# Performance work log

Measured on AMD Instinct MI355X. Metric: run time of the kernel, lower is better.

Reference implementation:

```python
import jax, jax.numpy as jnp
import numpy as np

N_GRAM = 3
N_HEAD = 8


def setup_inputs() -> dict:
    key = jax.random.key(0)
    ks = jax.random.split(key, 8)
    V, E, H, H2, C, B, L = 50000, 512, 512, 512, 10, 64, 512
    def rn(k, shape, scale):
        return jax.random.normal(k, shape, jnp.float32) * jnp.float32(scale)
    return {
        "x": jax.random.randint(ks[0], (B, L), 0, V),
        "emb": rn(ks[1], (V, E), 0.02),
        "Wq": rn(ks[2], (H, E), 1.0 / np.sqrt(H)),
        "Wx": rn(ks[3], (E, 3 * H), 1.0 / np.sqrt(E)),
        "Wh": rn(ks[4], (H, 3 * H), 1.0 / np.sqrt(H)),
        "bx": jnp.zeros((3 * H,), jnp.float32),
        "bh": jnp.zeros((3 * H,), jnp.float32),
        "W1": rn(ks[5], (H, H2), 1.0 / np.sqrt(H)),
        "b1": jnp.zeros((H2,), jnp.float32),
        "W2": rn(ks[6], (H2, C), 1.0 / np.sqrt(H2)),
        "b2": jnp.zeros((C,), jnp.float32),
    }


def _gru_ngram_attn(xe, Wq, Wx, Wh, bx, bh):
    # xe: [B, L, E] embedded sequence
    B, L, E = xe.shape
    g, nh = N_GRAM, N_HEAD
    hd = E // nh
    H = Wh.shape[0]
    scale = jnp.float32(1.0 / np.sqrt(hd))
    xpad = jnp.pad(xe, ((0, 0), (g - 1, 0), (0, 0)))
    win = jnp.stack([xpad[:, i:i + L] for i in range(g)], axis=2)  # [B,L,g,E]
    win_t = jnp.transpose(win, (1, 0, 2, 3))  # [L,B,g,E] for scan
    h0 = jnp.zeros((B, H), xe.dtype)

    def step(h, w):
        # multi-head dot attention: query from prev hidden, keys/values = n-gram window
        q = (h @ Wq).reshape(B, nh, hd)          # [B,nh,hd]
        k = w.reshape(B, g, nh, hd)              # [B,g,nh,hd]
        scores = jnp.einsum('bnd,bgnd->bng', q, k) * scale
        a = jax.nn.softmax(scores, axis=-1)      # over window positions
        ctx = jnp.einsum('bng,bgnd->bnd', a, k).reshape(B, E)
        # GRU cell with attended context as input
        gx = ctx @ Wx + bx
        gh = h @ Wh + bh
        xr, xz, xn = jnp.split(gx, 3, axis=-1)
        hr, hz, hn = jnp.split(gh, 3, axis=-1)
        r = jax.nn.sigmoid(xr + hr)
        z = jax.nn.sigmoid(xz + hz)
        n = jnp.tanh(xn + r * hn)
        hnew = (1.0 - z) * n + z * h
        return hnew, hnew

    _, hs = jax.lax.scan(step, h0, win_t)  # [L,B,H]
    return hs


def reference(x, emb, Wq, Wx, Wh, bx, bh, W1, b1, W2, b2):
    xe = emb[x]  # [B,L,E]
    hs = _gru_ngram_attn(xe, Wq, Wx, Wh, bx, bh)  # [L,B,H]
    pooled = jax.nn.relu(hs.sum(axis=0))          # sum over seq, then relu
    out = pooled @ W1 + b1                        # fc1 path (H != embed not needed; H is GRU out)
    out = out @ W2 + b2                           # [B,C]
    return out
```

## Files before the change

kernel.cpp:

```cpp
#include <hip/hip_runtime.h>
#include <hip/hip_fp16.h>

typedef __attribute__((ext_vector_type(2))) _Float16 half2v;
typedef __attribute__((ext_vector_type(2))) __fp16   fp16x2;

#define SEQ     512
#define THREADS 512

#define WQ_OFF   0
#define WX_OFF   32768
#define WH_OFF   131072
#define SYNC_OFF 3670016

__device__ inline unsigned int pack2f16(float a, float b) {
    fp16x2 p = __builtin_amdgcn_cvt_pkrtz(a, b);
    return __builtin_bit_cast(unsigned int, p);
}
__device__ inline float fdot2u(unsigned int a, unsigned int b, float acc) {
    return __builtin_amdgcn_fdot2(__builtin_bit_cast(half2v, a),
                                  __builtin_bit_cast(half2v, b), acc, false);
}
__device__ inline float dot4(uint4 h, uint4 w, float acc) {
    acc = fdot2u(h.x, w.x, acc); acc = fdot2u(h.y, w.y, acc);
    acc = fdot2u(h.z, w.z, acc); acc = fdot2u(h.w, w.w, acc);
    return acc;
}
__device__ inline float fsigmoid(float x) { return 1.f / (1.f + __expf(-x)); }
__device__ inline float ftanhf(float x) {
    float e = __expf(-2.f * fabsf(x));
    float t = (1.f - e) / (1.f + e);
    return copysignf(t, x);
}
__device__ inline void vmem_fence() { asm volatile("s_waitcnt vmcnt(0)" ::: "memory"); }
__device__ inline unsigned a_ld(unsigned* p) {
    return __hip_atomic_load(p, __ATOMIC_RELAXED, __HIP_MEMORY_SCOPE_AGENT);
}
__device__ inline void a_st(unsigned* p, unsigned v) {
    __hip_atomic_store(p, v, __ATOMIC_RELAXED, __HIP_MEMORY_SCOPE_AGENT);
}
__device__ inline float a_ldf(float* p) {
    return __hip_atomic_load(p, __ATOMIC_RELAXED, __HIP_MEMORY_SCOPE_AGENT);
}
__device__ inline void a_stf(float* p, float v) {
    __hip_atomic_store(p, v, __ATOMIC_RELAXED, __HIP_MEMORY_SCOPE_AGENT);
}

__global__ __launch_bounds__(256)
void pack_weights(const float* __restrict__ Wq,
                  const float* __restrict__ Wx,
                  const float* __restrict__ Wh,
                  uint4* __restrict__ ws) {
    int tid = blockIdx.x * blockDim.x + threadIdx.x;
    const float* src; uint4* dst; int C, idx;
    if (tid < 64 * 512)                  { src = Wq; dst = ws;          C = 512;  idx = tid; }
    else if (tid < 64 * 512 + 64 * 1536) { src = Wx; dst = ws + WX_OFF; C = 1536; idx = tid - 64 * 512; }
    else                                 { src = Wh; dst = ws + WH_OFF; C = 1536; idx = tid - (64 * 512 + 64 * 1536); }
    int m4 = idx / C;
    int c  = idx - m4 * C;
    const float* s = src + (size_t)(m4 * 8) * C + c;
    uint4 o;
    o.x = pack2f16(s[0 * (size_t)C], s[1 * (size_t)C]);
    o.y = pack2f16(s[2 * (size_t)C], s[3 * (size_t)C]);
    o.z = pack2f16(s[4 * (size_t)C], s[5 * (size_t)C]);
    o.w = pack2f16(s[6 * (size_t)C], s[7 * (size_t)C]);
    dst[idx] = o;
}

__global__ __launch_bounds__(THREADS)
void gru_scan(const int* __restrict__ xtok, const float* __restrict__ emb,
              const uint4* __restrict__ wsp, const float* __restrict__ bx,
              const float* __restrict__ bh, const float* __restrict__ W1,
              const float* __restrict__ b1, const float* __restrict__ W2,
              const float* __restrict__ b2, float* __restrict__ out)
{
    const int blk  = blockIdx.x;
    const int gid  = blk & 7;
    const int bid  = blk >> 3;
    const int tid  = threadIdx.x;
    const int lane = tid & 63;
    const int wid  = tid >> 6;
    const int colsub = lane & 7;
    const int bp     = (lane >> 3) & 3;
    const int chsub  = lane >> 5;

    char* syncb = (char*)wsp + SYNC_OFF;
    unsigned* flagH = (unsigned*)syncb;
    unsigned* flagS = (unsigned*)(syncb + 1024);
    unsigned* Hbuf  = (unsigned*)(syncb + 2048);
    float* Pbuf     = (float*)(syncb + 133120);
    float* pooled_g = (float*)(syncb + 182272);
    float* fc1_g    = (float*)(syncb + 313344);

    __shared__ uint4 lds_W [64][65];
    __shared__ uint4 lds_Wx[64][49];
    __shared__ uint4 lds_h4[8][65];
    __shared__ unsigned u_pk[3][8][48][4];
    __shared__ float redQf[1152];
    __shared__ float redH[8][48][9];
    __shared__ float a_all[8][8][3];

    for (int i = tid; i < 64 * 64; i += THREADS) {
        int ch = i >> 6, cl = i & 63;
        uint4 v;
        if (cl < 16) v = wsp[WQ_OFF + ch * 512 + bid * 16 + cl];
        else { int g = (cl - 16) >> 4, c = (cl - 16) & 15;
               v = wsp[WH_OFF + ch * 1536 + g * 512 + bid * 16 + c]; }
        lds_W[ch][cl] = v;
    }
    for (int i = tid; i < 64 * 48; i += THREADS) {
        int ch = i / 48, cl = i - ch * 48;
        int g = cl >> 4, c = cl & 15;
        lds_Wx[ch][cl] = wsp[WX_OFF + ch * 1536 + g * 512 + bid * 16 + c];
    }

    float bxr = 0, bxz = 0, bxn = 0, bhr = 0, bhz = 0, bhn = 0;
    if (tid < 128) {
        int c = tid >> 3, cg = bid * 16 + c;
        bxr = bx[cg]; bxz = bx[512 + cg]; bxn = bx[1024 + cg];
        bhr = bh[cg]; bhz = bh[512 + cg]; bhn = bh[1024 + cg];
    }

    const int gb = gid * 8 + wid;
    {
        int tk = xtok[gb * SEQ];
        const float4* p = (const float4*)(emb + (size_t)tk * 512 + lane * 8);
        float4 ra = p[0], rb = p[1];
        uint4 pk;
        pk.x = pack2f16(ra.x, ra.y); pk.y = pack2f16(ra.z, ra.w);
        pk.z = pack2f16(rb.x, rb.y); pk.w = pack2f16(rb.z, rb.w);
        lds_h4[wid][lane] = pk;
        unsigned* up = &u_pk[0][0][0][0];
        for (int i = tid; i < 3072; i += THREADS) up[1536 + i] = 0u;
    }
    float hprev = 0.f, pooledv = 0.f;
    __syncthreads();

    for (int t = 0; t < SEQ; ++t) {
        const int par = t & 1;
        const int slot = t % 3;

        int tnext = (t + 1 < SEQ) ? (t + 1) : t;
        int tkn = xtok[gb * SEQ + tnext];
        const float4* pn = (const float4*)(emb + (size_t)tkn * 512 + lane * 8);
        float4 r3a = pn[0], r3b = pn[1];

        float winv[16];
        int b3 = 0, g3 = 0, trow = -1;
        if (wid == 0 && lane < 24) {
            b3 = lane / 3; g3 = lane - b3 * 3;
            trow = t - 2 + g3;
            int tok = (trow >= 0) ? xtok[(gid * 8 + b3) * SEQ + trow] : -1;
            if (tok >= 0) {
                const float* er = emb + (size_t)tok * 512 + bid * 16;
                #pragma unroll
                for (int d = 0; d < 16; ++d) winv[d] = er[d];
            } else {
                #pragma unroll
                for (int d = 0; d < 16; ++d) winv[d] = 0.f;
            }
        }

        {
            float acu[12];
            #pragma unroll
            for (int i = 0; i < 12; ++i) acu[i] = 0.f;
            int ch0 = wid * 8 + chsub * 4;
            #pragma unroll
            for (int i = 0; i < 4; ++i) {
                int ch = ch0 + i;
                uint4 c0 = lds_h4[bp][ch], c1 = lds_h4[bp + 4][ch];
                #pragma unroll
                for (int j = 0; j < 6; ++j) {
                    uint4 w = lds_Wx[ch][colsub + 8 * j];
                    acu[j]     = dot4(c0, w, acu[j]);
                    acu[6 + j] = dot4(c1, w, acu[6 + j]);
                }
            }
            #pragma unroll
            for (int i = 0; i < 12; ++i) acu[i] += __shfl_xor(acu[i], 32);
            if (chsub == 0) {
                #pragma unroll
                for (int j = 0; j < 6; ++j)
                    u_pk[slot][wid][colsub + 8 * j][bp] = pack2f16(acu[j], acu[6 + j]);
            }
        }

        if (wid == 0) {
            bool done = lane >= 32;
            while (!__all(done)) {
                if (!done) done = (a_ld(&flagH[gid * 32 + lane]) >= (unsigned)t);
                if (!__all(done)) __builtin_amdgcn_s_sleep(1);
            }
        }
        __syncthreads();

        {
            int bb = tid >> 6, c4 = tid & 63;
            unsigned* s = Hbuf + (size_t)(par ^ 1) * 16384 + (gid * 8 + bb) * 256 + c4 * 4;
            uint4 v;
            v.x = a_ld(s); v.y = a_ld(s + 1); v.z = a_ld(s + 2); v.w = a_ld(s + 3);
            lds_h4[bb][c4] = v;
        }
        __syncthreads();

        {
            float aq0 = 0, aq1 = 0, aq2 = 0, aq3 = 0;
            int ch0 = wid * 8 + chsub * 4;
            #pragma unroll
            for (int i = 0; i < 4; ++i) {
                int ch = ch0 + i;
                uint4 h0 = lds_h4[bp][ch], h1 = lds_h4[bp + 4][ch];
                uint4 w0 = lds_W[ch][colsub], w1 = lds_W[ch][colsub + 8];
                aq0 = dot4(h0, w0, aq0); aq1 = dot4(h0, w1, aq1);
                aq2 = dot4(h1, w0, aq2); aq3 = dot4(h1, w1, aq3);
            }
            aq0 += __shfl_xor(aq0, 32); aq1 += __shfl_xor(aq1, 32);
            aq2 += __shfl_xor(aq2, 32); aq3 += __shfl_xor(aq3, 32);
            if (chsub == 0) {
                redQf[(wid * 16 + colsub) * 9 + bp]         = aq0;
                redQf[(wid * 16 + colsub + 8) * 9 + bp]     = aq1;
                redQf[(wid * 16 + colsub) * 9 + bp + 4]     = aq2;
                redQf[(wid * 16 + colsub + 8) * 9 + bp + 4] = aq3;
            }
        }
        __syncthreads();

        if (wid == 0) {
            if (lane < 24) {
                float s = 0.f;
                if (trow >= 0) {
                    #pragma unroll
                    for (int d = 0; d < 16; ++d) {
                        float q = redQf[d * 9 + b3];
                        #pragma unroll
                        for (int k = 1; k < 8; ++k) q += redQf[(k * 16 + d) * 9 + b3];
                        s += winv[d] * q;
                    }
                }
                a_stf(&Pbuf[(size_t)((par * 8 + gid) * 32 + bid) * 24 + b3 * 3 + g3], s);
            }
            vmem_fence();
            if (lane == 0) a_st(&flagS[gid * 32 + bid], (unsigned)(t + 1));
            bool done = lane >= 32;
            while (!__all(done)) {
                if (!done) done = (a_ld(&flagS[gid * 32 + lane]) >= (unsigned)(t + 1));
                if (!__all(done)) __builtin_amdgcn_s_sleep(1);
            }
            {
                int bb = lane >> 3, n = lane & 7;
                float* pb = Pbuf + (size_t)(par * 8 + gid) * 32 * 24;
                float sc0 = 0, sc1 = 0, sc2 = 0;
                #pragma unroll
                for (int j = 0; j < 4; ++j) {
                    float* pj = pb + (n * 4 + j) * 24 + bb * 3;
                    sc0 += a_ldf(pj); sc1 += a_ldf(pj + 1); sc2 += a_ldf(pj + 2);
                }
                sc0 *= 0.125f; sc1 *= 0.125f; sc2 *= 0.125f;
                float mx = fmaxf(sc0, fmaxf(sc1, sc2));
                float e0 = __expf(sc0 - mx), e1 = __expf(sc1 - mx), e2 = __expf(sc2 - mx);
                float inv = 1.f / (e0 + e1 + e2);
                a_all[bb][n][0] = e0 * inv; a_all[bb][n][1] = e1 * inv; a_all[bb][n][2] = e2 * inv;
            }
        } else {
            #pragma unroll 1
            for (int rep = 0; rep < 2; ++rep) {
                int k = (rep == 0) ? wid : 0;
                if (rep == 1 && wid != 7) break;
                float ag[12];
                #pragma unroll
                for (int i = 0; i < 12; ++i) ag[i] = 0.f;
                int ch0 = k * 8 + chsub * 4;
                #pragma unroll
                for (int i = 0; i < 4; ++i) {
                    int ch = ch0 + i;
                    uint4 h0 = lds_h4[bp][ch], h1 = lds_h4[bp + 4][ch];
                    #pragma unroll
                    for (int j = 0; j < 6; ++j) {
                        uint4 w = lds_W[ch][16 + colsub + 8 * j];
                        ag[j]     = dot4(h0, w, ag[j]);
                        ag[6 + j] = dot4(h1, w, ag[6 + j]);
                    }
                }
                #pragma unroll
                for (int i = 0; i < 12; ++i) ag[i] += __shfl_xor(ag[i], 32);
                if (chsub == 0) {
                    #pragma unroll
                    for (int j = 0; j < 6; ++j) {
                        redH[k][colsub + 8 * j][bp]     = ag[j];
                        redH[k][colsub + 8 * j][bp + 4] = ag[6 + j];
                    }
                }
            }
        }
        __syncthreads();

        if (tid >= 64 && tid < 448) {
            int idx = tid - 64;
            int col = idx >> 3, bb = idx & 7;
            float ghs = redH[0][col][bb];
            #pragma unroll
            for (int k = 1; k < 8; ++k) ghs += redH[k][col][bb];
            float gxs = 0.f;
            int half = bb >> 2, bq = bb & 3;
            #pragma unroll
            for (int g = 0; g < 3; ++g) {
                int sg = (t + 1 + g) % 3;
                #pragma unroll
                for (int k = 0; k < 8; ++k) {
                    fp16x2 uv = __builtin_bit_cast(fp16x2, u_pk[sg][k][col][bq]);
                    gxs += a_all[bb][k][g] * (float)uv[half];
                }
            }
            redQf[col * 8 + bb]       = ghs;
            redQf[384 + col * 8 + bb] = gxs;
        }
        {
            uint4 pk;
            pk.x = pack2f16(r3a.x, r3a.y); pk.y = pack2f16(r3a.z, r3a.w);
            pk.z = pack2f16(r3b.x, r3b.y); pk.w = pack2f16(r3b.z, r3b.w);
            lds_h4[wid][lane] = pk;
        }
        __syncthreads();

        if (tid < 128) {
            int c = tid >> 3, bb = tid & 7;
            float ghr = redQf[c * 8 + bb]        + bhr;
            float ghz = redQf[(16 + c) * 8 + bb] + bhz;
            float ghn = redQf[(32 + c) * 8 + bb] + bhn;
            float gxr = redQf[384 + c * 8 + bb]        + bxr;
            float gxz = redQf[384 + (16 + c) * 8 + bb] + bxz;
            float gxn = redQf[384 + (32 + c) * 8 + bb] + bxn;
            float r = fsigmoid(gxr + ghr);
            float z = fsigmoid(gxz + ghz);
            float n = ftanhf(gxn + r * ghn);
            float hnew = (1.f - z) * n + z * hprev;
            hprev = hnew; pooledv += hnew;
            float hnext = __shfl_down(hnew, 8);
            if ((c & 1) == 0)
                a_st(&Hbuf[(size_t)par * 16384 + (gid * 8 + bb) * 256 + bid * 8 + (c >> 1)],
                     pack2f16(hnew, hnext));
        }
        vmem_fence();
        __syncthreads();
        if (tid == 0) a_st(&flagH[gid * 32 + bid], (unsigned)(t + 1));
    }

    float* stage = (float*)&lds_W[0][0];
    if (tid < 128) {
        int c = tid >> 3, bb = tid & 7;
        a_stf(&pooled_g[(gid * 8 + bb) * 512 + bid * 16 + c], fmaxf(pooledv, 0.f));
    }
    vmem_fence();
    __syncthreads();
    if (tid == 0) a_st(&flagS[gid * 32 + bid], (unsigned)(SEQ + 1));
    if (wid == 0) {
        bool done = lane >= 32;
        while (!__all(done)) {
            if (!done) done = (a_ld(&flagS[gid * 32 + lane]) >= (unsigned)(SEQ + 1));
            if (!__all(done)) __builtin_amdgcn_s_sleep(1);
        }
    }
    __syncthreads();

    for (int i = tid; i < 8 * 512; i += THREADS) {
        int bb = i >> 9, k = i & 511;
        stage[bb * 512 + k] = a_ldf(&pooled_g[(gid * 8 + bb) * 512 + k]);
    }
    __syncthreads();

    if (tid < 128) {
        int c = tid >> 3, bb = tid & 7;
        int cg = bid * 16 + c;
        const float* pr = stage + bb * 512;
        float acc1 = b1[cg];
        for (int k = 0; k < 512; ++k) acc1 += pr[k] * W1[(size_t)k * 512 + cg];
        a_stf(&fc1_g[(gid * 8 + bb) * 512 + cg], acc1);
    }
    vmem_fence();
    __syncthreads();
    if (tid == 0) a_st(&flagH[gid * 32 + bid], (unsigned)(SEQ + 2));

    if (bid == 0) {
        if (wid == 0) {
            bool done = lane >= 32;
            while (!__all(done)) {
                if (!done) done = (a_ld(&flagH[gid * 32 + lane]) >= (unsigned)(SEQ + 2));
                if (!__all(done)) __builtin_amdgcn_s_sleep(1);
            }
        }
        __syncthreads();
        for (int i = tid; i < 8 * 512; i += THREADS) {
            int bb = i >> 9, k = i & 511;
            stage[bb * 512 + k] = a_ldf(&fc1_g[(gid * 8 + bb) * 512 + k]);
        }
        __syncthreads();
        if (tid < 80) {
            int bb = tid / 10, cls = tid - bb * 10;
            const float* fr = stage + bb * 512;
            float a2 = b2[cls];
            for (int k = 0; k < 512; ++k) a2 += fr[k] * W2[k * 10 + cls];
            out[(gid * 8 + bb) * 10 + cls] = a2;
        }
    }
}

extern "C" void kernel_launch(void* const* d_in, const int* in_sizes, int n_in,
                              void* d_out, int out_size, void* d_ws, size_t ws_size,
                              hipStream_t stream) {
    const int*   x   = (const int*)d_in[0];
    const float* emb = (const float*)d_in[1];
    const float* Wq  = (const float*)d_in[2];
    const float* Wx  = (const float*)d_in[3];
    const float* Wh  = (const float*)d_in[4];
    const float* bx  = (const float*)d_in[5];
    const float* bh  = (const float*)d_in[6];
    const float* W1  = (const float*)d_in[7];
    const float* b1  = (const float*)d_in[8];
    const float* W2  = (const float*)d_in[9];
    const float* b2  = (const float*)d_in[10];
    uint4* wsp = (uint4*)d_ws;
    float* outp = (float*)d_out;

    hipLaunchKernelGGL(pack_weights, dim3(896), dim3(256), 0, stream, Wq, Wx, Wh, wsp);
    hipMemsetAsync((char*)d_ws + SYNC_OFF, 0, 182272, stream);

    void* args[] = { (void*)&x, (void*)&emb, (void*)&wsp, (void*)&bx, (void*)&bh,
                     (void*)&W1, (void*)&b1, (void*)&W2, (void*)&b2, (void*)&outp };
    hipError_t e = hipLaunchCooperativeKernel((void*)gru_scan, dim3(256), dim3(THREADS),
                                              args, 0, stream);
    if (e != hipSuccess) {
        hipLaunchKernelGGL(gru_scan, dim3(256), dim3(THREADS), 0, stream,
                           x, emb, wsp, bx, bh, W1, b1, W2, b2, outp);
    }
}
```

Baseline: 3.621 ms.

## Shorten per-step critical path: warp 0 owns GRU update and flag, others prefetch

Reorganises the per-timestep work in the persistent GRU scan. Wave 0 now only spins on the cross-block flag while waves 1-7 compute the input-projection partials and prefetch the next embeddings. Wave 0 alone does the gate nonlinearity for two columns per lane and publishes the flag directly, which removes one block-wide barrier per step. The Q partial reduction is switched to LDS atomicAdd into a small buffer instead of an 8-way serial sum. The cost is uneven load across waves (wave 7 and wave 1 take extra work), plus the LDS atomic contention and the extra zeroing of that buffer.

```diff
diff --git a/kernel.cpp b/kernel.cpp
--- a/kernel.cpp
+++ b/kernel.cpp
@@ -78,7 +78,7 @@
     const int bid  = blk >> 3;
     const int tid  = threadIdx.x;
     const int lane = tid & 63;
-    const int wid  = tid >> 6;
+    const int w    = tid >> 6;
     const int colsub = lane & 7;
     const int bp     = (lane >> 3) & 3;
     const int chsub  = lane >> 5;
@@ -95,8 +95,9 @@
     __shared__ uint4 lds_Wx[64][49];
     __shared__ uint4 lds_h4[8][65];
     __shared__ unsigned u_pk[3][8][48][4];
-    __shared__ float redQf[1152];
     __shared__ float redH[8][48][9];
+    __shared__ float redC[768];
+    __shared__ float redQsum[144];
     __shared__ float a_all[8][8][3];
 
     for (int i = tid; i < 64 * 64; i += THREADS) {
@@ -113,40 +114,59 @@
         lds_Wx[ch][cl] = wsp[WX_OFF + ch * 1536 + g * 512 + bid * 16 + c];
     }
 
-    float bxr = 0, bxz = 0, bxn = 0, bhr = 0, bhz = 0, bhn = 0;
-    if (tid < 128) {
-        int c = tid >> 3, cg = bid * 16 + c;
-        bxr = bx[cg]; bxz = bx[512 + cg]; bxn = bx[1024 + cg];
-        bhr = bh[cg]; bhz = bh[512 + cg]; bhn = bh[1024 + cg];
-    }
-
-    const int gb = gid * 8 + wid;
+    float bhr0 = 0, bhr1 = 0, bhz0 = 0, bhz1 = 0, bhn0 = 0, bhn1 = 0;
+    float bxr0 = 0, bxr1 = 0, bxz0 = 0, bxz1 = 0, bxn0 = 0, bxn1 = 0;
+    if (w == 0) {
+        int cg = bid * 16 + (lane & 7) * 2;
+        bhr0 = bh[cg];        bhr1 = bh[cg + 1];
+        bhz0 = bh[512 + cg];  bhz1 = bh[513 + cg];
+        bhn0 = bh[1024 + cg]; bhn1 = bh[1025 + cg];
+        bxr0 = bx[cg];        bxr1 = bx[cg + 1];
+        bxz0 = bx[512 + cg];  bxz1 = bx[513 + cg];
+        bxn0 = bx[1024 + cg]; bxn1 = bx[1025 + cg];
+    }
+
+    if (w >= 1) {
+        #pragma unroll 1
+        for (int rep = 0; rep < 2; ++rep) {
+            if (rep == 1 && w != 1) break;
+            int bd = (rep == 0) ? w : 0;
+            int tk = xtok[(gid * 8 + bd) * SEQ];
+            const float4* p = (const float4*)(emb + (size_t)tk * 512 + lane * 8);
+            float4 ra = p[0], rb = p[1];
+            uint4 pk;
+            pk.x = pack2f16(ra.x, ra.y); pk.y = pack2f16(ra.z, ra.w);
+            pk.z = pack2f16(rb.x, rb.y); pk.w = pack2f16(rb.z, rb.w);
+            lds_h4[bd][lane] = pk;
+        }
+    }
     {
-        int tk = xtok[gb * SEQ];
-        const float4* p = (const float4*)(emb + (size_t)tk * 512 + lane * 8);
-        float4 ra = p[0], rb = p[1];
-        uint4 pk;
-        pk.x = pack2f16(ra.x, ra.y); pk.y = pack2f16(ra.z, ra.w);
-        pk.z = pack2f16(rb.x, rb.y); pk.w = pack2f16(rb.z, rb.w);
-        lds_h4[wid][lane] = pk;
         unsigned* up = &u_pk[0][0][0][0];
         for (int i = tid; i < 3072; i += THREADS) up[1536 + i] = 0u;
     }
-    float hprev = 0.f, pooledv = 0.f;
+    float hp0 = 0.f, hp1 = 0.f, pv0 = 0.f, pv1 = 0.f;
     __syncthreads();
 
     for (int t = 0; t < SEQ; ++t) {
-        const int par = t & 1;
-        const int slot = t % 3;
-
-        int tnext = (t + 1 < SEQ) ? (t + 1) : t;
-        int tkn = xtok[gb * SEQ + tnext];
-        const float4* pn = (const float4*)(emb + (size_t)tkn * 512 + lane * 8);
-        float4 r3a = pn[0], r3b = pn[1];
+        const int par   = t & 1;
+        const int uslot = t % 3;
+
+        float4 r3a0, r3b0, r3a1, r3b1;
+        if (w >= 1) {
+            int tn = (t + 1 < SEQ) ? t + 1 : t;
+            int tk = xtok[(gid * 8 + w) * SEQ + tn];
+            const float4* pn = (const float4*)(emb + (size_t)tk * 512 + lane * 8);
+            r3a0 = pn[0]; r3b0 = pn[1];
+            if (w == 1) {
+                int tk0 = xtok[(gid * 8 + 0) * SEQ + tn];
+                const float4* p0 = (const float4*)(emb + (size_t)tk0 * 512 + lane * 8);
+                r3a1 = p0[0]; r3b1 = p0[1];
+            }
+        }
 
         float winv[16];
         int b3 = 0, g3 = 0, trow = -1;
-        if (wid == 0 && lane < 24) {
+        if (w == 0 && lane < 24) {
             b3 = lane / 3; g3 = lane - b3 * 3;
             trow = t - 2 + g3;
             int tok = (trow >= 0) ? xtok[(gid * 8 + b3) * SEQ + trow] : -1;
@@ -160,52 +180,56 @@
             }
         }
 
-        {
-            float acu[12];
-            #pragma unroll
-            for (int i = 0; i < 12; ++i) acu[i] = 0.f;
-            int ch0 = wid * 8 + chsub * 4;
-            #pragma unroll
-            for (int i = 0; i < 4; ++i) {
-                int ch = ch0 + i;
-                uint4 c0 = lds_h4[bp][ch], c1 = lds_h4[bp + 4][ch];
-                #pragma unroll
-                for (int j = 0; j < 6; ++j) {
-                    uint4 w = lds_Wx[ch][colsub + 8 * j];
-                    acu[j]     = dot4(c0, w, acu[j]);
-                    acu[6 + j] = dot4(c1, w, acu[6 + j]);
-                }
-            }
-            #pragma unroll
-            for (int i = 0; i < 12; ++i) acu[i] += __shfl_xor(acu[i], 32);
-            if (chsub == 0) {
-                #pragma unroll
-                for (int j = 0; j < 6; ++j)
-                    u_pk[slot][wid][colsub + 8 * j][bp] = pack2f16(acu[j], acu[6 + j]);
-            }
-        }
-
-        if (wid == 0) {
+        if (w == 0) {
             bool done = lane >= 32;
             while (!__all(done)) {
                 if (!done) done = (a_ld(&flagH[gid * 32 + lane]) >= (unsigned)t);
                 if (!__all(done)) __builtin_amdgcn_s_sleep(1);
             }
+        } else {
+            #pragma unroll 1
+            for (int rep = 0; rep < 2; ++rep) {
+                int k = (rep == 0) ? w : 0;
+                if (rep == 1 && w != 7) break;
+                float acu[12];
+                #pragma unroll
+                for (int i = 0; i < 12; ++i) acu[i] = 0.f;
+                int ch0 = k * 8 + chsub * 4;
+                #pragma unroll
+                for (int i = 0; i < 4; ++i) {
+                    int ch = ch0 + i;
+                    uint4 c0 = lds_h4[bp][ch], c1 = lds_h4[bp + 4][ch];
+                    #pragma unroll
+                    for (int j = 0; j < 6; ++j) {
+                        uint4 wv = lds_Wx[ch][colsub + 8 * j];
+                        acu[j]     = dot4(c0, wv, acu[j]);
+                        acu[6 + j] = dot4(c1, wv, acu[6 + j]);
+                    }
+                }
+                #pragma unroll
+                for (int i = 0; i < 12; ++i) acu[i] += __shfl_xor(acu[i], 32);
+                if (chsub == 0) {
+                    #pragma unroll
+                    for (int j = 0; j < 6; ++j)
+                        u_pk[uslot][k][colsub + 8 * j][bp] = pack2f16(acu[j], acu[6 + j]);
+                }
+            }
         }
         __syncthreads();
 
         {
-            int bb = tid >> 6, c4 = tid & 63;
-            unsigned* s = Hbuf + (size_t)(par ^ 1) * 16384 + (gid * 8 + bb) * 256 + c4 * 4;
+            int bb = tid >> 6, ch = tid & 63;
+            unsigned* s = Hbuf + (size_t)(par ^ 1) * 16384 + (gid * 8 + bb) * 256 + ch * 4;
             uint4 v;
             v.x = a_ld(s); v.y = a_ld(s + 1); v.z = a_ld(s + 2); v.w = a_ld(s + 3);
-            lds_h4[bb][c4] = v;
-        }
+            lds_h4[bb][ch] = v;
+        }
+        if (tid < 144) redQsum[tid] = 0.f;
         __syncthreads();
 
         {
             float aq0 = 0, aq1 = 0, aq2 = 0, aq3 = 0;
-            int ch0 = wid * 8 + chsub * 4;
+            int ch0 = w * 8 + chsub * 4;
             #pragma unroll
             for (int i = 0; i < 4; ++i) {
                 int ch = ch0 + i;
@@ -217,25 +241,20 @@
             aq0 += __shfl_xor(aq0, 32); aq1 += __shfl_xor(aq1, 32);
             aq2 += __shfl_xor(aq2, 32); aq3 += __shfl_xor(aq3, 32);
             if (chsub == 0) {
-                redQf[(wid * 16 + colsub) * 9 + bp]         = aq0;
-                redQf[(wid * 16 + colsub + 8) * 9 + bp]     = aq1;
-                redQf[(wid * 16 + colsub) * 9 + bp + 4]     = aq2;
-                redQf[(wid * 16 + colsub + 8) * 9 + bp + 4] = aq3;
-            }
-        }
-        __syncthreads();
-
-        if (wid == 0) {
+                atomicAdd(&redQsum[colsub * 9 + bp], aq0);
+                atomicAdd(&redQsum[(colsub + 8) * 9 + bp], aq1);
+                atomicAdd(&redQsum[colsub * 9 + bp + 4], aq2);
+                atomicAdd(&redQsum[(colsub + 8) * 9 + bp + 4], aq3);
+            }
+        }
+        __syncthreads();
+
+        if (w == 0) {
             if (lane < 24) {
                 float s = 0.f;
                 if (trow >= 0) {
                     #pragma unroll
-                    for (int d = 0; d < 16; ++d) {
-                        float q = redQf[d * 9 + b3];
-                        #pragma unroll
-                        for (int k = 1; k < 8; ++k) q += redQf[(k * 16 + d) * 9 + b3];
-                        s += winv[d] * q;
-                    }
+                    for (int d = 0; d < 16; ++d) s += winv[d] * redQsum[d * 9 + b3];
                 }
                 a_stf(&Pbuf[(size_t)((par * 8 + gid) * 32 + bid) * 24 + b3 * 3 + g3], s);
             }
@@ -264,8 +283,8 @@
         } else {
             #pragma unroll 1
             for (int rep = 0; rep < 2; ++rep) {
-                int k = (rep == 0) ? wid : 0;
-                if (rep == 1 && wid != 7) break;
+                int k = (rep == 0) ? w : 0;
+                if (rep == 1 && w != 7) break;
                 float ag[12];
                 #pragma unroll
                 for (int i = 0; i < 12; ++i) ag[i] = 0.f;
@@ -276,9 +295,9 @@
                     uint4 h0 = lds_h4[bp][ch], h1 = lds_h4[bp + 4][ch];
                     #pragma unroll
                     for (int j = 0; j < 6; ++j) {
-                        uint4 w = lds_W[ch][16 + colsub + 8 * j];
-                        ag[j]     = dot4(h0, w, ag[j]);
-                        ag[6 + j] = dot4(h1, w, ag[6 + j]);
+                        uint4 wv = lds_W[ch][16 + colsub + 8 * j];
+                        ag[j]     = dot4(h0, wv, ag[j]);
+                        ag[6 + j] = dot4(h1, wv, ag[6 + j]);
                     }
                 }
                 #pragma unroll
@@ -297,10 +316,10 @@
         if (tid >= 64 && tid < 448) {
             int idx = tid - 64;
             int col = idx >> 3, bb = idx & 7;
-            float ghs = redH[0][col][bb];
+            float ghsum = redH[0][col][bb];
             #pragma unroll
-            for (int k = 1; k < 8; ++k) ghs += redH[k][col][bb];
-            float gxs = 0.f;
+            for (int k = 1; k < 8; ++k) ghsum += redH[k][col][bb];
+            float gxsum = 0.f;
             int half = bb >> 2, bq = bb & 3;
             #pragma unroll
             for (int g = 0; g < 3; ++g) {
@@ -308,52 +327,55 @@
                 #pragma unroll
                 for (int k = 0; k < 8; ++k) {
                     fp16x2 uv = __builtin_bit_cast(fp16x2, u_pk[sg][k][col][bq]);
-                    gxs += a_all[bb][k][g] * (float)uv[half];
-                }
-            }
-            redQf[col * 8 + bb]       = ghs;
-            redQf[384 + col * 8 + bb] = gxs;
-        }
-        {
+                    gxsum += a_all[bb][k][g] * (float)uv[half];
+                }
+            }
+            redC[col * 8 + bb]       = ghsum;
+            redC[384 + col * 8 + bb] = gxsum;
+        }
+        if (w >= 1) {
             uint4 pk;
-            pk.x = pack2f16(r3a.x, r3a.y); pk.y = pack2f16(r3a.z, r3a.w);
-            pk.z = pack2f16(r3b.x, r3b.y); pk.w = pack2f16(r3b.z, r3b.w);
-            lds_h4[wid][lane] = pk;
-        }
-        __syncthreads();
-
-        if (tid < 128) {
-            int c = tid >> 3, bb = tid & 7;
-            float ghr = redQf[c * 8 + bb]        + bhr;
-            float ghz = redQf[(16 + c) * 8 + bb] + bhz;
-            float ghn = redQf[(32 + c) * 8 + bb] + bhn;
-            float gxr = redQf[384 + c * 8 + bb]        + bxr;
-            float gxz = redQf[384 + (16 + c) * 8 + bb] + bxz;
-            float gxn = redQf[384 + (32 + c) * 8 + bb] + bxn;
-            float r = fsigmoid(gxr + ghr);
-            float z = fsigmoid(gxz + ghz);
-            float n = ftanhf(gxn + r * ghn);
-            float hnew = (1.f - z) * n + z * hprev;
-            hprev = hnew; pooledv += hnew;
-            float hnext = __shfl_down(hnew, 8);
-            if ((c & 1) == 0)
-                a_st(&Hbuf[(size_t)par * 16384 + (gid * 8 + bb) * 256 + bid * 8 + (c >> 1)],
-                     pack2f16(hnew, hnext));
-        }
+            pk.x = pack2f16(r3a0.x, r3a0.y); pk.y = pack2f16(r3a0.z, r3a0.w);
+            pk.z = pack2f16(r3b0.x, r3b0.y); pk.w = pack2f16(r3b0.z, r3b0.w);
+            lds_h4[w][lane] = pk;
+            if (w == 1) {
+                uint4 pk1;
+                pk1.x = pack2f16(r3a1.x, r3a1.y); pk1.y = pack2f16(r3a1.z, r3a1.w);
+                pk1.z = pack2f16(r3b1.x, r3b1.y); pk1.w = pack2f16(r3b1.z, r3b1.w);
+                lds_h4[0][lane] = pk1;
+            }
+        }
+        __syncthreads();
+
+        if (w == 0) {
+            int bb = lane >> 3, cp = lane & 7;
+            int c0 = cp * 2, c1 = c0 + 1;
+            float r0 = fsigmoid(redC[384 + c0 * 8 + bb] + bxr0 + redC[c0 * 8 + bb] + bhr0);
+            float z0 = fsigmoid(redC[384 + (16 + c0) * 8 + bb] + bxz0 + redC[(16 + c0) * 8 + bb] + bhz0);
+            float n0 = ftanhf(redC[384 + (32 + c0) * 8 + bb] + bxn0 + r0 * (redC[(32 + c0) * 8 + bb] + bhn0));
+            float h0 = (1.f - z0) * n0 + z0 * hp0;
+            float r1 = fsigmoid(redC[384 + c1 * 8 + bb] + bxr1 + redC[c1 * 8 + bb] + bhr1);
+            float z1 = fsigmoid(redC[384 + (16 + c1) * 8 + bb] + bxz1 + redC[(16 + c1) * 8 + bb] + bhz1);
+            float n1 = ftanhf(redC[384 + (32 + c1) * 8 + bb] + bxn1 + r1 * (redC[(32 + c1) * 8 + bb] + bhn1));
+            float h1 = (1.f - z1) * n1 + z1 * hp1;
+            hp0 = h0; hp1 = h1; pv0 += h0; pv1 += h1;
+            a_st(&Hbuf[(size_t)par * 16384 + (gid * 8 + bb) * 256 + bid * 8 + cp],
+                 pack2f16(h0, h1));
+            vmem_fence();
+            if (lane == 0) a_st(&flagH[gid * 32 + bid], (unsigned)(t + 1));
+        }
+    }
+
+    float* stage = (float*)&lds_W[0][0];
+    if (w == 0) {
+        int bb = lane >> 3, cp = lane & 7;
+        a_stf(&pooled_g[(gid * 8 + bb) * 512 + bid * 16 + cp * 2],     fmaxf(pv0, 0.f));
+        a_stf(&pooled_g[(gid * 8 + bb) * 512 + bid * 16 + cp * 2 + 1], fmaxf(pv1, 0.f));
         vmem_fence();
-        __syncthreads();
-        if (tid == 0) a_st(&flagH[gid * 32 + bid], (unsigned)(t + 1));
-    }
-
-    float* stage = (float*)&lds_W[0][0];
-    if (tid < 128) {
-        int c = tid >> 3, bb = tid & 7;
-        a_stf(&pooled_g[(gid * 8 + bb) * 512 + bid * 16 + c], fmaxf(pooledv, 0.f));
-    }
-    vmem_fence();
+    }
     __syncthreads();
     if (tid == 0) a_st(&flagS[gid * 32 + bid], (unsigned)(SEQ + 1));
-    if (wid == 0) {
+    if (w == 0) {
         bool done = lane >= 32;
         while (!__all(done)) {
             if (!done) done = (a_ld(&flagS[gid * 32 + lane]) >= (unsigned)(SEQ + 1));
@@ -381,7 +403,7 @@
     if (tid == 0) a_st(&flagH[gid * 32 + bid], (unsigned)(SEQ + 2));
 
     if (bid == 0) {
-        if (wid == 0) {
+        if (w == 0) {
             bool done = lane >= 32;
             while (!__all(done)) {
                 if (!done) done = (a_ld(&flagH[gid * 32 + lane]) >= (unsigned)(SEQ + 2));
```

Result: slower. 4.037 ms (+11.5%).
